# Kernel tuning notes

Measured on AMD Instinct MI355X. Metric: run time of the kernel, lower is better.

## Reference

```python
import jax, jax.numpy as jnp
import numpy as np

B, T, D, K = 8, 4096, 1024, 3


def setup_inputs() -> dict:
    key = jax.random.key(0)
    k0, k1, k2 = jax.random.split(key, 3)
    x = jax.random.normal(k0, (B, T, D), dtype=jnp.float32)
    lim = 1.0 / np.sqrt(D)
    Wv = jax.random.uniform(k1, (D, D), dtype=jnp.float32, minval=-lim, maxval=lim)
    bv = jnp.zeros((D,), dtype=jnp.float32)
    Wo = jax.random.uniform(k2, (D, D), dtype=jnp.float32, minval=-lim, maxval=lim)
    bo = jnp.zeros((D,), dtype=jnp.float32)
    neighbor_weights = jnp.ones((K,), dtype=jnp.float32) / K
    return {"x": x, "Wv": Wv, "bv": bv, "Wo": Wo, "bo": bo,
            "neighbor_weights": neighbor_weights}


def reference(x, Wv, bv, Wo, bo, neighbor_weights):
    # x: [B, T, D]; faithful translation of the unfold -> Linear -> weighted-sum chain
    k = neighbor_weights.shape[0]
    pad = k // 2
    t = x.shape[1]
    # replicate padding along T (torch F.pad mode='replicate')
    xp = jnp.pad(x, ((0, 0), (pad, pad), (0, 0)), mode='edge')  # [B, T+2*pad, D]
    # sliding windows: [B, T, K, D] (small fixed K loop, not a data-dim loop)
    windows = jnp.stack([xp[:, i:i + t, :] for i in range(k)], axis=2)
    # value projection applied per window element (nn.Linear: x @ W.T + b)
    v = jnp.einsum('btkd,ed->btke', windows, Wv) + bv  # [B, T, K, D]
    # fixed-weight neighbor average
    attended = jnp.einsum('btkd,k->btd', v, neighbor_weights)  # [B, T, D]
    # output projection
    return jnp.einsum('btd,ed->bte', attended, Wo) + bo
```

## Files before the change

### kernel.cpp

```cpp
#include <hip/hip_runtime.h>
#include <stdint.h>
#include <stddef.h>

typedef _Float16 f16_t;
typedef _Float16 f16x4 __attribute__((ext_vector_type(4)));
typedef _Float16 f16x8 __attribute__((ext_vector_type(8)));
typedef float f32x4 __attribute__((ext_vector_type(4)));
typedef float f32x8 __attribute__((ext_vector_type(8)));

#define AS_G __attribute__((address_space(1)))
#define AS_L __attribute__((address_space(3)))

__device__ __forceinline__ void gload_lds16(const void* g, void* l) {
  __builtin_amdgcn_global_load_lds((AS_G void*)g, (AS_L void*)l, 16, 0, 0);
}

#define FENCE() asm volatile("" ::: "memory")
#define BARX()                            \
  do {                                    \
    FENCE();                              \
    __builtin_amdgcn_s_barrier();         \
    FENCE();                              \
  } while (0)
#define VMCNT(n) asm volatile("s_waitcnt vmcnt(" #n ")" ::: "memory")
#define LGKM0() asm volatile("s_waitcnt lgkmcnt(0)" ::: "memory")
#if defined(__HIP_DEVICE_COMPILE__)
#define SCHEDB0() __builtin_amdgcn_sched_barrier(0)
#else
#define SCHEDB0()
#endif


__global__ __launch_bounds__(256) void prep_fused_kernel(
    const float* __restrict__ X, const float* __restrict__ Wo,
    const float* __restrict__ Wv, const float* __restrict__ bv,
    const float* __restrict__ bo, const float* __restrict__ nw, int Kw,
    f16_t* __restrict__ Xavg, f16_t* __restrict__ WcT, float* __restrict__ bc) {
  __shared__ __align__(16) f16_t sA[128 * 32];
  __shared__ __align__(16) float sWvT[128 * 36];
  __shared__ float smem[256];
  const int b = blockIdx.x;
  const int tid = threadIdx.x;

  if (b < 64) {
    constexpr int K = 1024, NN = 1024;
    const int mt = b & 7, nt = b >> 3;
    const int m0 = mt << 7, n0 = nt << 7;
    const int l = tid & 63, w = tid >> 6;
    const int wr = w >> 1, wc = w & 1;
    const int q = l >> 4;
    const int ka = q << 3;
    const int ar = (wr << 6) + (l & 15);
    const int br = (wc << 6) + (l & 15);
    const int kS = tid >> 3;
    const int cS = (tid & 7) << 4;

    f32x4 acc[4][4];
#pragma unroll
    for (int i = 0; i < 4; ++i)
#pragma unroll
      for (int j = 0; j < 4; ++j) acc[i][j] = f32x4{0.f, 0.f, 0.f, 0.f};

    for (int kt = 0; kt < (K >> 5); ++kt) {
      const int kb = kt << 5;
#pragma unroll
      for (int i = 0; i < 2; ++i) {
        const int u = tid + i * 256;
        const int row = u >> 2, ch = u & 3;
        f32x8 v = *(const f32x8*)(Wo + (size_t)(m0 + row) * K + kb + ch * 8);
        f16x8 h;
#pragma unroll
        for (int e = 0; e < 8; ++e) h[e] = (f16_t)v[e];
        *(f16x8*)(sA + row * 32 + ch * 8) = h;
      }
#pragma unroll
      for (int j = 0; j < 4; ++j) {
        f32x4 v = *(const f32x4*)(Wv + (size_t)(kb + kS) * NN + n0 + cS + 4 * j);
#pragma unroll
        for (int i = 0; i < 4; ++i) sWvT[(cS + 4 * j + i) * 36 + kS] = v[i];
      }
      __syncthreads();
      f16x8 af[4], bfr[4];
#pragma unroll
      for (int m = 0; m < 4; ++m) af[m] = *(const f16x8*)(sA + (ar + (m << 4)) * 32 + ka);
#pragma unroll
      for (int n = 0; n < 4; ++n) {
        f32x4 v0 = *(const f32x4*)(sWvT + (br + (n << 4)) * 36 + ka);
        f32x4 v1 = *(const f32x4*)(sWvT + (br + (n << 4)) * 36 + ka + 4);
#pragma unroll
        for (int e = 0; e < 4; ++e) {
          bfr[n][e] = (f16_t)v0[e];
          bfr[n][e + 4] = (f16_t)v1[e];
        }
      }
#pragma unroll
      for (int m = 0; m < 4; ++m)
#pragma unroll
        for (int n = 0; n < 4; ++n)
          acc[m][n] = __builtin_amdgcn_mfma_f32_16x16x32_f16(af[m], bfr[n], acc[m][n], 0, 0, 0);
      __syncthreads();
    }

    const int orow = q << 2;
    const int ocol = l & 15;
#pragma unroll
    for (int n = 0; n < 4; ++n) {
      const int gn = n0 + (wc << 6) + (n << 4) + ocol;
#pragma unroll
      for (int m = 0; m < 4; ++m) {
        const int gm = m0 + (wr << 6) + (m << 4) + orow;
#pragma unroll
        for (int j = 0; j < 4; ++j)
          WcT[(size_t)(gm + j) * NN + gn] = (f16_t)acc[m][n][j];
      }
    }
  } else if (b < 1088) {
    const int e = b - 64;
    float sw = 0.f;
    for (int k = 0; k < Kw; ++k) sw += nw[k];
    float p = 0.f;
    for (int d = tid; d < 1024; d += 256) p += Wo[(size_t)e * 1024 + d] * bv[d];
    smem[tid] = p;
    __syncthreads();
    for (int s = 128; s > 0; s >>= 1) {
      if (tid < s) smem[tid] += smem[tid + s];
      __syncthreads();
    }
    if (tid == 0) bc[e] = sw * smem[0] + bo[e];
  } else {
    const int T = 4096, D = 1024;
    const int base = (b - 1088) * 8;
    const int bb = (base >> 12) << 12;
    const int be = bb + T - 1;
    const int half = tid >> 7;
    const int r0 = base + (half << 2);
    const int col = (tid & 127) << 3;
    const float w0 = nw[0], w1 = nw[1], w2 = nw[2];
    const float* xb = X + (size_t)r0 * D + col;
    f32x8 pp = *(const f32x8*)(xb + ((r0 == bb) ? 0 : -D));
    f32x8 pc = *(const f32x8*)(xb);
    f16_t* ob = Xavg + (size_t)r0 * D + col;
#pragma unroll
    for (int g = 0; g < 4; ++g) {
      f32x8 pn;
      if (r0 + g == be) pn = pc;
      else pn = *(const f32x8*)(xb + (size_t)(g + 1) * D);
      f32x8 y = w0 * pp + w1 * pc + w2 * pn;
      f16x8 o;
#pragma unroll
      for (int e = 0; e < 8; ++e) o[e] = (f16_t)y[e];
      *(f16x8*)(ob + (size_t)g * D) = o;
      pp = pc;
      pc = pn;
    }
  }
}


__device__ __forceinline__ void stageA64(const f16_t* __restrict__ Ap, int K, int kt,
                                         int c, char* bufA, int w, int l) {
  const int f = w * 64 + l;
  const int sub = f >> 3, ch = f & 7;
  const int grow = ((c & 1) << 7) + ((c >> 1) << 6) + sub;
  const int gcol = (kt << 6) + ((ch ^ (sub & 7)) << 3);
  gload_lds16(Ap + (size_t)grow * K + gcol, bufA + c * 8192 + w * 1024);
}

__device__ __forceinline__ void stageB64(const f16_t* __restrict__ Bp, int K, int kt,
                                         int c, char* bufB, int w, int l) {
  const int f = w * 64 + l;
  const int rr = f >> 3, ch = f & 7;
  const int wc = ((c & 1) << 1) + (rr >> 5);
  const int sub = rr & 31;
  const int grow = (wc << 6) + ((c >> 1) << 5) + sub;
  const int gcol = (kt << 6) + ((ch ^ (sub & 7)) << 3);
  gload_lds16(Bp + (size_t)grow * K + gcol, bufB + c * 8192 + w * 1024);
}

__global__ __launch_bounds__(512, 2) void gemm8p_kernel(const f16_t* __restrict__ A,
                                                        const f16_t* __restrict__ Bt,
                                                        float* __restrict__ C,
                                                        const float* __restrict__ bias,
                                                        int M, int N, int K) {
  __shared__ __align__(16) char lds[2 * 65536];
  const int tid = threadIdx.x;
  const int l = tid & 63;
  const int w = tid >> 6;
  const int wr = w >> 2;
  const int wc = w & 3;
  const int lr = l & 15;
  const int q = l >> 4;

  const int cpx = (int)gridDim.x >> 3;
  const int swzb = ((int)blockIdx.x & 7) * cpx + ((int)blockIdx.x >> 3);
  const int nNT = N >> 8;
  const int mt = swzb / nNT;
  const int nt = swzb % nNT;
  const int m0 = mt << 8;
  const int n0 = nt << 8;

  const f16_t* Apanel = A + (size_t)m0 * K;
  const f16_t* Bpanel = Bt + (size_t)n0 * K;

  const int x7 = lr & 7;

  f32x4 acc[8][4];
#pragma unroll
  for (int m = 0; m < 8; ++m)
#pragma unroll
    for (int n = 0; n < 4; ++n) acc[m][n] = f32x4{0.f, 0.f, 0.f, 0.f};

  const int nT = K >> 6;

  f16x8 a0[4][2], a1[4][2], b0[2][2], b1[2][2];

#define AREAD(DST, MH, BUF)                                                     \
  do {                                                                          \
    const char* p_ = (BUF) + (((MH)*2 + wr) << 13);                             \
    _Pragma("unroll") for (int mm = 0; mm < 4; ++mm)                            \
      _Pragma("unroll") for (int kk = 0; kk < 2; ++kk)                          \
        DST[mm][kk] = *(const f16x8*)(p_ + ((mm * 16 + lr) << 7) +              \
                                      ((((kk << 2) + q) ^ x7) << 4));           \
  } while (0)
#define BREAD(DST, NP, BUF)                                                     \
  do {                                                                          \
    const char* p_ = (BUF) + 32768 + ((((NP) << 2) + wc) << 12);                \
    _Pragma("unroll") for (int nn = 0; nn < 2; ++nn)                            \
      _Pragma("unroll") for (int kk = 0; kk < 2; ++kk)                          \
        DST[nn][kk] = *(const f16x8*)(p_ + ((nn * 16 + lr) << 7) +              \
                                      ((((kk << 2) + q) ^ x7) << 4));           \
  } while (0)
#define PH_MFMA(MB, AR, BR, NPB)                                                \
  do {                                                                          \
    __builtin_amdgcn_s_setprio(1);                                              \
    _Pragma("unroll") for (int mm = 0; mm < 4; ++mm)                            \
      _Pragma("unroll") for (int nn = 0; nn < 2; ++nn) {                        \
        acc[(MB) + mm][(NPB)*2 + nn] = __builtin_amdgcn_mfma_f32_16x16x32_f16(  \
            AR[mm][0], BR[nn][0], acc[(MB) + mm][(NPB)*2 + nn], 0, 0, 0);       \
        acc[(MB) + mm][(NPB)*2 + nn] = __builtin_amdgcn_mfma_f32_16x16x32_f16(  \
            AR[mm][1], BR[nn][1], acc[(MB) + mm][(NPB)*2 + nn], 0, 0, 0);       \
      }                                                                         \
    __builtin_amdgcn_s_setprio(0);                                              \
  } while (0)

  stageA64(Apanel, K, 0, 0, lds, w, l);
  stageB64(Bpanel, K, 0, 0, lds + 32768, w, l);
  stageA64(Apanel, K, 0, 1, lds, w, l);
  stageB64(Bpanel, K, 0, 1, lds + 32768, w, l);
  stageA64(Apanel, K, 0, 2, lds, w, l);
  stageB64(Bpanel, K, 0, 2, lds + 32768, w, l);
  stageA64(Apanel, K, 0, 3, lds, w, l);
  stageB64(Bpanel, K, 0, 3, lds + 32768, w, l);
  VMCNT(4);
  BARX();

  for (int tt = 0; tt < nT; ++tt) {
    char* cur = lds + (tt & 1) * 65536;
    char* nxtA = lds + ((tt + 1) & 1) * 65536;
    char* nxtB = nxtA + 32768;
    const int ktn = (tt + 1) < nT ? (tt + 1) : (nT - 1);

    AREAD(a0, 0, cur);
    BREAD(b0, 0, cur);
    stageA64(Apanel, K, ktn, 0, nxtA, w, l);
    stageB64(Bpanel, K, ktn, 0, nxtB, w, l);
    VMCNT(2);
    BARX();
    LGKM0();
    SCHEDB0();
    PH_MFMA(0, a0, b0, 0);
    BARX();

    BREAD(b1, 1, cur);
    stageA64(Apanel, K, ktn, 1, nxtA, w, l);
    stageB64(Bpanel, K, ktn, 1, nxtB, w, l);
    BARX();
    LGKM0();
    SCHEDB0();
    PH_MFMA(0, a0, b1, 1);
    BARX();

    AREAD(a1, 1, cur);
    stageA64(Apanel, K, ktn, 2, nxtA, w, l);
    stageB64(Bpanel, K, ktn, 2, nxtB, w, l);
    BARX();
    LGKM0();
    SCHEDB0();
    PH_MFMA(4, a1, b0, 0);
    BARX();

    stageA64(Apanel, K, ktn, 3, nxtA, w, l);
    stageB64(Bpanel, K, ktn, 3, nxtB, w, l);
    BARX();
    PH_MFMA(4, a1, b1, 1);
    VMCNT(4);
    BARX();
  }
#undef AREAD
#undef BREAD
#undef PH_MFMA

  float bs[4];
#pragma unroll
  for (int n = 0; n < 4; ++n) bs[n] = bias[n0 + (wc << 6) + (n << 4) + lr];
#pragma unroll
  for (int m = 0; m < 8; ++m) {
    const int gm = m0 + (wr << 7) + (m << 4) + (q << 2);
#pragma unroll
    for (int j = 0; j < 4; ++j) {
      float* Crow = C + (size_t)(gm + j) * N + n0 + (wc << 6) + lr;
#pragma unroll
      for (int n = 0; n < 4; ++n) Crow[n << 4] = acc[m][n][j] + bs[n];
    }
  }
}


extern "C" void kernel_launch(void* const* d_in, const int* in_sizes, int n_in,
                              void* d_out, int out_size, void* d_ws, size_t ws_size,
                              hipStream_t stream) {
  const float* x = (const float*)d_in[0];
  const float* Wv = (const float*)d_in[1];
  const float* bv = (const float*)d_in[2];
  const float* Wo = (const float*)d_in[3];
  const float* bo = (const float*)d_in[4];
  const float* nw = (const float*)d_in[5];
  float* out = (float*)d_out;

  char* ws = (char*)d_ws;
  f16_t* WcT  = (f16_t*)(ws + (4u << 20));
  float* bc   = (float*)(ws + (6u << 20));
  f16_t* Xavg = (f16_t*)(ws + (8u << 20));

  prep_fused_kernel<<<dim3(5184), dim3(256), 0, stream>>>(
      x, Wo, Wv, bv, bo, nw, in_sizes[5], Xavg, WcT, bc);
  gemm8p_kernel<<<dim3(512), dim3(512), 0, stream>>>(
      Xavg, WcT, out, bc, 32768, 1024, 1024);
}
```

Before: 139.9 us.

## Split weight conversion/transpose into a pre-kernel and feed combined-weight GEMM via direct LDS loads

Converting Wo to fp16 and transposing Wv to fp16 now happen in a separate pre-pass kernel, which also computes the bias. The 64-block Wo·Wv GEMM then streams both operands with global_load_lds straight into shared memory, with no in-loop fp32-to-fp16 conversion and no scattered transpose writes. The Xavg blocks now handle 32 rows each instead of 8, giving fewer and larger blocks. The cost is an extra kernel launch and a round trip of the weights through workspace memory.

```diff
diff --git a/kernel.cpp b/kernel.cpp
--- a/kernel.cpp
+++ b/kernel.cpp
@@ -31,68 +31,98 @@
 #endif
 
 
-__global__ __launch_bounds__(256) void prep_fused_kernel(
-    const float* __restrict__ X, const float* __restrict__ Wo,
-    const float* __restrict__ Wv, const float* __restrict__ bv,
-    const float* __restrict__ bo, const float* __restrict__ nw, int Kw,
-    f16_t* __restrict__ Xavg, f16_t* __restrict__ WcT, float* __restrict__ bc) {
-  __shared__ __align__(16) f16_t sA[128 * 32];
-  __shared__ __align__(16) float sWvT[128 * 36];
-  __shared__ float smem[256];
+__global__ __launch_bounds__(256) void wprep_kernel(
+    const float* __restrict__ Wo, const float* __restrict__ Wv,
+    const float* __restrict__ bv, const float* __restrict__ bo,
+    const float* __restrict__ nw, int Kw,
+    f16_t* __restrict__ Wo_h, f16_t* __restrict__ WvT, float* __restrict__ bc) {
+  __shared__ float smem[32 * 33];
+  const int b = blockIdx.x;
+  const int t = threadIdx.x;
+  if (b < 1024) {
+    const int i = b * 256 + t;
+    f32x4 v = ((const f32x4*)Wo)[i];
+    f16x4 o;
+    o.x = (f16_t)v.x; o.y = (f16_t)v.y; o.z = (f16_t)v.z; o.w = (f16_t)v.w;
+    ((f16x4*)Wo_h)[i] = o;
+  } else if (b < 2048) {
+    const int i = b - 1024;
+    const int bx = i & 31, by = i >> 5;
+    const int tx = t & 31, ty = t >> 5;
+#pragma unroll
+    for (int k = 0; k < 32; k += 8)
+      smem[(ty + k) * 33 + tx] = Wv[(size_t)(by * 32 + ty + k) * 1024 + bx * 32 + tx];
+    __syncthreads();
+#pragma unroll
+    for (int k = 0; k < 32; k += 8)
+      WvT[(size_t)(bx * 32 + ty + k) * 1024 + by * 32 + tx] = (f16_t)smem[tx * 33 + ty + k];
+  } else {
+    const int e = b - 2048;
+    float sw = 0.f;
+    for (int k = 0; k < Kw; ++k) sw += nw[k];
+    float p = 0.f;
+    for (int d = t; d < 1024; d += 256) p += Wo[(size_t)e * 1024 + d] * bv[d];
+    smem[t] = p;
+    __syncthreads();
+    for (int s = 128; s > 0; s >>= 1) {
+      if (t < s) smem[t] += smem[t + s];
+      __syncthreads();
+    }
+    if (t == 0) bc[e] = sw * smem[0] + bo[e];
+  }
+}
+
+
+__global__ __launch_bounds__(256) void xavg_wct_kernel(
+    const float* __restrict__ X, const float* __restrict__ nw,
+    const f16_t* __restrict__ Wo_h, const f16_t* __restrict__ WvT,
+    f16_t* __restrict__ Xavg, f16_t* __restrict__ WcT) {
+  __shared__ __align__(16) f16_t sAB[2 * 128 * 32];
   const int b = blockIdx.x;
   const int tid = threadIdx.x;
 
   if (b < 64) {
     constexpr int K = 1024, NN = 1024;
-    const int mt = b & 7, nt = b >> 3;
-    const int m0 = mt << 7, n0 = nt << 7;
-    const int l = tid & 63, w = tid >> 6;
-    const int wr = w >> 1, wc = w & 1;
-    const int q = l >> 4;
-    const int ka = q << 3;
+    f16_t* sA = sAB;
+    f16_t* sB = sAB + 128 * 32;
+    const int l = tid & 63;
+    const int w = tid >> 6;
+    const int wr = w >> 1;
+    const int wc = w & 1;
+    const int mt = b & 7;
+    const int nt = b >> 3;
+    const int m0 = mt << 7;
+    const int n0 = nt << 7;
+
+    const int srow = (w << 4) + (l >> 2);
+    const int scol = (l & 3) << 3;
+    const size_t aoff0 = (size_t)(m0 + srow) * K + scol;
+    const size_t boff0 = (size_t)(n0 + srow) * K + scol;
+    f16_t* ldsA = sA + (w << 9);
+    f16_t* ldsB = sB + (w << 9);
+
+    f32x4 acc[4][4];
+#pragma unroll
+    for (int i = 0; i < 4; ++i)
+#pragma unroll
+      for (int j = 0; j < 4; ++j) acc[i][j] = f32x4{0.f, 0.f, 0.f, 0.f};
+
+    const int ka = (l >> 4) << 3;
     const int ar = (wr << 6) + (l & 15);
     const int br = (wc << 6) + (l & 15);
-    const int kS = tid >> 3;
-    const int cS = (tid & 7) << 4;
-
-    f32x4 acc[4][4];
-#pragma unroll
-    for (int i = 0; i < 4; ++i)
-#pragma unroll
-      for (int j = 0; j < 4; ++j) acc[i][j] = f32x4{0.f, 0.f, 0.f, 0.f};
 
     for (int kt = 0; kt < (K >> 5); ++kt) {
       const int kb = kt << 5;
-#pragma unroll
-      for (int i = 0; i < 2; ++i) {
-        const int u = tid + i * 256;
-        const int row = u >> 2, ch = u & 3;
-        f32x8 v = *(const f32x8*)(Wo + (size_t)(m0 + row) * K + kb + ch * 8);
-        f16x8 h;
-#pragma unroll
-        for (int e = 0; e < 8; ++e) h[e] = (f16_t)v[e];
-        *(f16x8*)(sA + row * 32 + ch * 8) = h;
-      }
-#pragma unroll
-      for (int j = 0; j < 4; ++j) {
-        f32x4 v = *(const f32x4*)(Wv + (size_t)(kb + kS) * NN + n0 + cS + 4 * j);
-#pragma unroll
-        for (int i = 0; i < 4; ++i) sWvT[(cS + 4 * j + i) * 36 + kS] = v[i];
-      }
+      gload_lds16(Wo_h + aoff0 + kb, ldsA);
+      gload_lds16(Wo_h + aoff0 + ((size_t)K << 6) + kb, ldsA + 2048);
+      gload_lds16(WvT + boff0 + kb, ldsB);
+      gload_lds16(WvT + boff0 + ((size_t)K << 6) + kb, ldsB + 2048);
       __syncthreads();
       f16x8 af[4], bfr[4];
 #pragma unroll
-      for (int m = 0; m < 4; ++m) af[m] = *(const f16x8*)(sA + (ar + (m << 4)) * 32 + ka);
-#pragma unroll
-      for (int n = 0; n < 4; ++n) {
-        f32x4 v0 = *(const f32x4*)(sWvT + (br + (n << 4)) * 36 + ka);
-        f32x4 v1 = *(const f32x4*)(sWvT + (br + (n << 4)) * 36 + ka + 4);
-#pragma unroll
-        for (int e = 0; e < 4; ++e) {
-          bfr[n][e] = (f16_t)v0[e];
-          bfr[n][e + 4] = (f16_t)v1[e];
-        }
-      }
+      for (int m = 0; m < 4; ++m) af[m] = *(const f16x8*)(sA + ((ar + (m << 4)) << 5) + ka);
+#pragma unroll
+      for (int n = 0; n < 4; ++n) bfr[n] = *(const f16x8*)(sB + ((br + (n << 4)) << 5) + ka);
 #pragma unroll
       for (int m = 0; m < 4; ++m)
 #pragma unroll
@@ -101,7 +131,7 @@
       __syncthreads();
     }
 
-    const int orow = q << 2;
+    const int orow = (l >> 4) << 2;
     const int ocol = l & 15;
 #pragma unroll
     for (int n = 0; n < 4; ++n) {
@@ -114,26 +144,13 @@
           WcT[(size_t)(gm + j) * NN + gn] = (f16_t)acc[m][n][j];
       }
     }
-  } else if (b < 1088) {
-    const int e = b - 64;
-    float sw = 0.f;
-    for (int k = 0; k < Kw; ++k) sw += nw[k];
-    float p = 0.f;
-    for (int d = tid; d < 1024; d += 256) p += Wo[(size_t)e * 1024 + d] * bv[d];
-    smem[tid] = p;
-    __syncthreads();
-    for (int s = 128; s > 0; s >>= 1) {
-      if (tid < s) smem[tid] += smem[tid + s];
-      __syncthreads();
-    }
-    if (tid == 0) bc[e] = sw * smem[0] + bo[e];
   } else {
     const int T = 4096, D = 1024;
-    const int base = (b - 1088) * 8;
-    const int bb = (base >> 12) << 12;
+    const int R0 = (b - 64) * 32;
+    const int half = tid >> 7;
+    const int r0 = R0 + (half << 4);
+    const int bb = (r0 >> 12) << 12;
     const int be = bb + T - 1;
-    const int half = tid >> 7;
-    const int r0 = base + (half << 2);
     const int col = (tid & 127) << 3;
     const float w0 = nw[0], w1 = nw[1], w2 = nw[2];
     const float* xb = X + (size_t)r0 * D + col;
@@ -141,7 +158,7 @@
     f32x8 pc = *(const f32x8*)(xb);
     f16_t* ob = Xavg + (size_t)r0 * D + col;
 #pragma unroll
-    for (int g = 0; g < 4; ++g) {
+    for (int g = 0; g < 16; ++g) {
       f32x8 pn;
       if (r0 + g == be) pn = pc;
       else pn = *(const f32x8*)(xb + (size_t)(g + 1) * D);
@@ -328,12 +345,16 @@
   float* out = (float*)d_out;
 
   char* ws = (char*)d_ws;
+  f16_t* Wo_h = (f16_t*)(ws);
+  f16_t* WvT  = (f16_t*)(ws + (2u << 20));
   f16_t* WcT  = (f16_t*)(ws + (4u << 20));
   float* bc   = (float*)(ws + (6u << 20));
   f16_t* Xavg = (f16_t*)(ws + (8u << 20));
 
-  prep_fused_kernel<<<dim3(5184), dim3(256), 0, stream>>>(
-      x, Wo, Wv, bv, bo, nw, in_sizes[5], Xavg, WcT, bc);
+  wprep_kernel<<<dim3(3072), dim3(256), 0, stream>>>(
+      Wo, Wv, bv, bo, nw, in_sizes[5], Wo_h, WvT, bc);
+  xavg_wct_kernel<<<dim3(1088), dim3(256), 0, stream>>>(
+      x, nw, Wo_h, WvT, Xavg, WcT);
   gemm8p_kernel<<<dim3(512), dim3(512), 0, stream>>>(
       Xavg, WcT, out, bc, 32768, 1024, 1024);
 }
```

New measurement: 134.0 us (median of 2 runs). 1.04x faster.
